# Kernel optimization log

Hardware: AMD Instinct MI355X
Metric: run time of the kernel (lower is better)

## Reference

```python
import jax, jax.numpy as jnp
import numpy as np
import math

B, T, C = 2, 2048, 2048
H, G, HS = 16, 4, 128  # n_head, n_query_groups, head_size
EPS = 1e-5
SCALE = 1.0 / math.sqrt(HS)
QKV_DIM = (H + 2 * G) * HS  # 3072, gate logits (H) appended after


def _build_rope(seq_len, n_elem, base):
    freq = base ** (np.arange(0, n_elem, 2, dtype=np.float64) / n_elem)
    inv_freq = 1.0 / freq
    idx_theta = np.outer(np.arange(seq_len, dtype=np.float64), inv_freq)
    return (jnp.asarray(np.cos(idx_theta), dtype=jnp.float32),
            jnp.asarray(np.sin(idx_theta), dtype=jnp.float32))


def setup_inputs() -> dict:
    key = jax.random.key(0)
    k1, k2, k3 = jax.random.split(key, 3)
    x = jax.random.normal(k1, (B, T, C), dtype=jnp.float32)
    # rope base per module: 0.09 * local_window ** 1.628
    base = 0.09 * (2048.0 ** 1.628)
    cos, sin = _build_rope(T, HS, base)  # [T, HS//2]
    W_attn = jax.random.normal(k2, (QKV_DIM + H, C), dtype=jnp.float32) * 0.02
    W_proj = jax.random.normal(k3, (C, H * HS), dtype=jnp.float32) * 0.02
    q_norm_w = jnp.ones((HS,), dtype=jnp.float32)
    k_norm_w = jnp.ones((HS,), dtype=jnp.float32)
    return {"x": x, "cos": cos, "sin": sin, "W_attn": W_attn,
            "q_norm_w": q_norm_w, "k_norm_w": k_norm_w, "W_proj": W_proj}


def _rms_norm(v, w):
    # per-head RMSNorm over last dim (head_size)
    ms = jnp.mean(jnp.square(v), axis=-1, keepdims=True)
    return v * jax.lax.rsqrt(ms + EPS) * w


def _apply_rope(v, cos, sin):
    # v: [B, T, N, HS]; cos/sin: [T, HS//2]; non-interleaved halves
    d2 = v.shape[-1] // 2
    x1, x2 = v[..., :d2], v[..., d2:]
    c = cos[None, :, None, :]
    s = sin[None, :, None, :]
    return jnp.concatenate([x1 * c - x2 * s, x2 * c + x1 * s], axis=-1)


def reference(x, cos, sin, W_attn, q_norm_w, k_norm_w, W_proj):
    qkv = jnp.einsum('btc,oc->bto', x, W_attn)  # [B, T, QKV_DIM+H]
    q = qkv[..., : H * HS].reshape(B, T, H, HS)
    k = qkv[..., H * HS:(H + G) * HS].reshape(B, T, G, HS)
    v = qkv[..., (H + G) * HS: QKV_DIM].reshape(B, T, G, HS)
    gate = qkv[..., QKV_DIM:]  # [B, T, H]

    q = _apply_rope(_rms_norm(q, q_norm_w), cos, sin)
    k = _apply_rope(_rms_norm(k, k_norm_w), cos, sin)

    rep = H // G
    kr = jnp.repeat(k, rep, axis=2)  # [B, T, H, HS]
    vr = jnp.repeat(v, rep, axis=2)

    scores = jnp.einsum('bthd,bshd->bhts', q, kr) * SCALE  # [B, H, T, T]
    causal = jnp.tril(jnp.ones((T, T), dtype=bool))
    scores = jnp.where(causal, scores, jnp.finfo(scores.dtype).min)
    probs = jax.nn.softmax(scores, axis=-1)
    out = jnp.einsum('bhts,bshd->bthd', probs, vr)  # [B, T, H, HS]

    out = out * jax.nn.sigmoid(gate)[..., None]  # gated attention, per-head
    y = jnp.einsum('bto,co->btc', out.reshape(B, T, H * HS), W_proj)
    return y
```

## Files before the change

### kernel.cpp

```cpp
#include <hip/hip_runtime.h>

#define T_   2048
#define BB   2
#define CC   2048
#define HH   16
#define GG   4
#define HSS  128
#define QKVD 3072
#define NQKV 3088
#define NPAD 3200
#define SCALE_ 0.08838834764831845f

typedef __attribute__((ext_vector_type(8))) short  short8;
typedef __attribute__((ext_vector_type(4))) float  f32x4;
typedef __attribute__((ext_vector_type(4))) int    v4i;
typedef __attribute__((ext_vector_type(4))) float  v4f;
typedef __attribute__((ext_vector_type(4))) unsigned short u16x4;

typedef const void __attribute__((address_space(1)))* gas1_t;
typedef void __attribute__((address_space(3)))* as3_t;

__device__ __forceinline__ void gl_lds16(const void* g, void* l) {
    __builtin_amdgcn_global_load_lds((gas1_t)g, (as3_t)l, 16, 0, 0);
}

__device__ __forceinline__ unsigned short f2bf(float f) {
    unsigned u = __float_as_uint(f);
    u += 0x7fffu + ((u >> 16) & 1u);
    return (unsigned short)(u >> 16);
}
__device__ __forceinline__ float bf2f(unsigned short h) {
    return __uint_as_float(((unsigned)h) << 16);
}

__global__ void k_convert(const float* __restrict__ src, unsigned short* __restrict__ dst,
                          int n_src4, int n_dst4) {
    int i = blockIdx.x * blockDim.x + threadIdx.x;
    if (i >= n_dst4) return;
    u16x4 o;
    if (i < n_src4) {
        v4f v = *(const v4f*)(src + (size_t)i * 4);
        o[0] = f2bf(v[0]); o[1] = f2bf(v[1]); o[2] = f2bf(v[2]); o[3] = f2bf(v[3]);
    } else {
        o[0] = 0; o[1] = 0; o[2] = 0; o[3] = 0;
    }
    *(u16x4*)(dst + (size_t)i * 4) = o;
}

template <typename OutT>
__launch_bounds__(512, 2)
__global__ void k_gemm8(const unsigned short* __restrict__ A,
                        const unsigned short* __restrict__ Bm,
                        OutT* __restrict__ C,
                        int K, int lda, int ldb, int ldc, int nmax) {
    __shared__ unsigned short As[2][256 * 64];
    __shared__ unsigned short Bs[2][256 * 64];
    const int t = threadIdx.x;
    const int lane = t & 63;
    const int wid  = t >> 6;
    const int wr = wid >> 2, wc = wid & 3;
    const int bm = blockIdx.x, bn = blockIdx.y;
    const int fro = lane & 15, fk = lane >> 4;

    const int srow  = lane >> 3;
    const size_t scol = (size_t)(((lane & 7) ^ srow) * 8);

    const unsigned short* Abase = A  + (size_t)(bm * 256) * lda;
    const unsigned short* Bbase = Bm + (size_t)(bn * 256) * ldb;

    f32x4 acc[8][4];
#pragma unroll
    for (int i = 0; i < 8; ++i)
#pragma unroll
        for (int j = 0; j < 4; ++j) acc[i][j] = (f32x4){0.f, 0.f, 0.f, 0.f};

#pragma unroll
    for (int h = 0; h < 2; ++h)
#pragma unroll
        for (int c8 = 0; c8 < 2; ++c8) {
            const int rr = h * 128 + wid * 16 + c8 * 8;
            gl_lds16(Abase + (size_t)(rr + srow) * lda + scol, &As[0][rr * 64]);
            gl_lds16(Bbase + (size_t)(rr + srow) * ldb + scol, &Bs[0][rr * 64]);
        }

    int cur = 0;
    for (int kt = 0; kt < K; kt += 64) {
        asm volatile("s_waitcnt vmcnt(0)" ::: "memory");
        __builtin_amdgcn_s_barrier();
        __builtin_amdgcn_sched_barrier(0);
        const bool pf = (kt + 64 < K);
        const int nxt = cur ^ 1;
        const int kn = kt + 64;

        short8 bf_[4][2];
#pragma unroll
        for (int q = 0; q < 4; ++q) {
            short8 af[2][2];
#pragma unroll
            for (int im = 0; im < 2; ++im)
#pragma unroll
                for (int kk = 0; kk < 2; ++kk) {
                    const int ar = wr * 128 + (q * 2 + im) * 16 + fro;
                    af[im][kk] = *(const short8*)&As[cur][ar * 64 + ((kk * 4 + fk) ^ (ar & 7)) * 8];
                }
            if (q == 0) {
#pragma unroll
                for (int ni = 0; ni < 4; ++ni)
#pragma unroll
                    for (int kk = 0; kk < 2; ++kk) {
                        const int br = wc * 64 + ni * 16 + fro;
                        bf_[ni][kk] = *(const short8*)&Bs[cur][br * 64 + ((kk * 4 + fk) ^ (br & 7)) * 8];
                    }
            }
            if (pf) {
                const int h = q & 1;
#pragma unroll
                for (int c8 = 0; c8 < 2; ++c8) {
                    const int rr = h * 128 + wid * 16 + c8 * 8;
                    if ((q >> 1) == 0)
                        gl_lds16(Abase + (size_t)(rr + srow) * lda + kn + scol, &As[nxt][rr * 64]);
                    else
                        gl_lds16(Bbase + (size_t)(rr + srow) * ldb + kn + scol, &Bs[nxt][rr * 64]);
                }
            }
            __builtin_amdgcn_s_setprio(1);
#pragma unroll
            for (int im = 0; im < 2; ++im)
#pragma unroll
                for (int ni = 0; ni < 4; ++ni)
#pragma unroll
                    for (int kk = 0; kk < 2; ++kk)
                        acc[q * 2 + im][ni] = __builtin_amdgcn_mfma_f32_16x16x32_bf16(
                            af[im][kk], bf_[ni][kk], acc[q * 2 + im][ni], 0, 0, 0);
            __builtin_amdgcn_s_setprio(0);
            __builtin_amdgcn_s_barrier();
        }
        cur ^= 1;
    }

    const int col16 = lane & 15, rbase = (lane >> 4) * 4;
    const int gr0 = bm * 256 + wr * 128;
    const int gc0 = bn * 256 + wc * 64;
#pragma unroll
    for (int mi = 0; mi < 8; ++mi)
#pragma unroll
        for (int ni = 0; ni < 4; ++ni) {
            const int gcol = gc0 + ni * 16 + col16;
            if (gcol < nmax) {
#pragma unroll
                for (int r = 0; r < 4; ++r) {
                    const int grow = gr0 + mi * 16 + rbase + r;
                    float v = acc[mi][ni][r];
                    if constexpr (sizeof(OutT) == 2)
                        C[(size_t)grow * ldc + gcol] = (OutT)f2bf(v);
                    else
                        C[(size_t)grow * ldc + gcol] = (OutT)v;
                }
            }
        }
}

__global__ void k_normrope(unsigned short* __restrict__ qkv,
                           const float* __restrict__ cosT, const float* __restrict__ sinT,
                           const float* __restrict__ qw, const float* __restrict__ kw) {
    const int lane = threadIdx.x & 63;
    const int row  = blockIdx.x * 4 + (threadIdx.x >> 6);
    const int tok  = row / 20;
    const int hh   = row - tok * 20;
    const int tpos = tok & (T_ - 1);
    unsigned short* rp = qkv + (size_t)tok * NPAD + (hh < 16 ? hh * 128 : 2048 + (hh - 16) * 128);
    const float* w = (hh < 16) ? qw : kw;
    float e1 = bf2f(rp[lane]);
    float e2 = bf2f(rp[lane + 64]);
    float ss = e1 * e1 + e2 * e2;
#pragma unroll
    for (int m = 1; m < 64; m <<= 1) ss += __shfl_xor(ss, m);
    float inv = rsqrtf(ss * (1.0f / 128.0f) + 1e-5f);
    float n1 = e1 * inv * w[lane];
    float n2 = e2 * inv * w[lane + 64];
    float c = cosT[tpos * 64 + lane];
    float s = sinT[tpos * 64 + lane];
    rp[lane]      = f2bf(n1 * c - n2 * s);
    rp[lane + 64] = f2bf(n2 * c + n1 * s);
}

__global__ void k_transposeV(const unsigned short* __restrict__ qkv,
                             unsigned short* __restrict__ vt) {
    __shared__ unsigned short tile[64][65];
    const int b = blockIdx.x >> 2, g = blockIdx.x & 3;
    const int s0 = blockIdx.y * 64, d0 = blockIdx.z * 64;
    const int tx = threadIdx.x & 63, ty0 = threadIdx.x >> 6;
    const unsigned short* src = qkv + (size_t)(b * T_ + s0) * NPAD + 2560 + g * 128 + d0;
#pragma unroll
    for (int r = 0; r < 16; ++r) {
        int ty = ty0 * 16 + r;
        tile[ty][tx] = src[(size_t)ty * NPAD + tx];
    }
    __syncthreads();
    unsigned short* dstp = vt + ((size_t)(b * GG + g) * 128 + d0) * T_ + s0;
#pragma unroll
    for (int r = 0; r < 16; ++r) {
        int ty = ty0 * 16 + r;
        dstp[(size_t)ty * T_ + tx] = tile[tx][ty];
    }
}

__launch_bounds__(256, 2)
__global__ void k_attn(const unsigned short* __restrict__ qkv,
                       const unsigned short* __restrict__ vt,
                       unsigned short* __restrict__ ao) {
    __shared__ unsigned short Ks[2][64 * 128];
    __shared__ unsigned short Vs[2][128 * 64];
    __shared__ unsigned short Ps[4][16 * 72];
    const int t = threadIdx.x;
    const int lane = t & 63;
    const int wid  = t >> 6;
    const int id = blockIdx.x;
    const int bg = id & 7;
    const int hh = (id >> 3) & 3;
    const int pr = id >> 5;
    const int b = bg >> 2, g = bg & 3, h = g * 4 + hh;
    const int fro = lane & 15, fk = lane >> 4;
    const int rbase = fk * 4;

    const unsigned short* kg0 = qkv + (size_t)(b * T_) * NPAD + 2048 + g * 128;
    const unsigned short* vg0 = vt + (size_t)(b * GG + g) * 128 * T_;

    const int cp0 = wid * 4;
    int cur = 0;

#pragma unroll
    for (int seg = 0; seg < 2; ++seg) {
        const int qt = (seg == 0) ? pr : 31 - pr;
        const int q0w = qt * 64 + wid * 16;

        short8 qf[4];
        const unsigned short* qp = qkv + (size_t)(b * T_ + q0w + fro) * NPAD + h * 128 + fk * 8;
#pragma unroll
        for (int kb = 0; kb < 4; ++kb) qf[kb] = *(const short8*)(qp + kb * 32);

        float m_r[4], l_r[4];
        f32x4 o[8];
#pragma unroll
        for (int r = 0; r < 4; ++r) { m_r[r] = -1e30f; l_r[r] = 0.f; }
#pragma unroll
        for (int d = 0; d < 8; ++d) o[d] = (f32x4){0.f, 0.f, 0.f, 0.f};

        const int nt = qt + 1;

#pragma unroll
        for (int p = 0; p < 4; ++p) {
            const int cp = cp0 + p;
            const int kr = cp * 4 + (lane >> 4);
            const int sK = lane & 15;
            gl_lds16(kg0 + (size_t)kr * NPAD + (size_t)((sK ^ (kr & 7)) * 8), &Ks[cur][cp * 512]);
            const int d  = cp * 8 + (lane >> 3);
            const int sV = lane & 7;
            gl_lds16(vg0 + (size_t)d * T_ + (size_t)((sV ^ (d & 7)) * 8), &Vs[cur][cp * 512]);
        }
        __syncthreads();

        for (int ti = 0; ti < nt; ++ti) {
            if (ti + 1 < nt) {
                const int sn = (ti + 1) * 64;
#pragma unroll
                for (int p = 0; p < 4; ++p) {
                    const int cp = cp0 + p;
                    const int kr = cp * 4 + (lane >> 4);
                    const int sK = lane & 15;
                    gl_lds16(kg0 + (size_t)(sn + kr) * NPAD + (size_t)((sK ^ (kr & 7)) * 8), &Ks[cur ^ 1][cp * 512]);
                    const int d  = cp * 8 + (lane >> 3);
                    const int sV = lane & 7;
                    gl_lds16(vg0 + (size_t)d * T_ + sn + (size_t)((sV ^ (d & 7)) * 8), &Vs[cur ^ 1][cp * 512]);
                }
            }
            f32x4 sc[4];
#pragma unroll
            for (int jb = 0; jb < 4; ++jb) sc[jb] = (f32x4){0.f, 0.f, 0.f, 0.f};
#pragma unroll
            for (int jb = 0; jb < 4; ++jb) {
                const int kr = jb * 16 + fro;
#pragma unroll
                for (int kb = 0; kb < 4; ++kb) {
                    short8 kf = *(const short8*)&Ks[cur][kr * 128 + 8 * ((kb * 4 + fk) ^ (kr & 7))];
                    sc[jb] = __builtin_amdgcn_mfma_f32_16x16x32_bf16(qf[kb], kf, sc[jb], 0, 0, 0);
                }
            }
            const bool domask = (ti == qt);
#pragma unroll
            for (int jb = 0; jb < 4; ++jb)
#pragma unroll
                for (int r = 0; r < 4; ++r) {
                    float v = sc[jb][r] * SCALE_;
                    if (domask && (jb * 16 + fro) > (wid * 16 + rbase + r)) v = -1e30f;
                    sc[jb][r] = v;
                }
            float mx[4], fs[4], rs[4];
#pragma unroll
            for (int r = 0; r < 4; ++r)
                mx[r] = fmaxf(fmaxf(sc[0][r], sc[1][r]), fmaxf(sc[2][r], sc[3][r]));
#pragma unroll
            for (int msk = 1; msk < 16; msk <<= 1)
#pragma unroll
                for (int r = 0; r < 4; ++r) mx[r] = fmaxf(mx[r], __shfl_xor(mx[r], msk));
#pragma unroll
            for (int r = 0; r < 4; ++r) {
                float mn = fmaxf(m_r[r], mx[r]);
                fs[r] = __expf(m_r[r] - mn);
                m_r[r] = mn;
            }
#pragma unroll
            for (int jb = 0; jb < 4; ++jb)
#pragma unroll
                for (int r = 0; r < 4; ++r) sc[jb][r] = __expf(sc[jb][r] - m_r[r]);
#pragma unroll
            for (int r = 0; r < 4; ++r)
                rs[r] = (sc[0][r] + sc[1][r]) + (sc[2][r] + sc[3][r]);
#pragma unroll
            for (int msk = 1; msk < 16; msk <<= 1)
#pragma unroll
                for (int r = 0; r < 4; ++r) rs[r] += __shfl_xor(rs[r], msk);
#pragma unroll
            for (int r = 0; r < 4; ++r) l_r[r] = l_r[r] * fs[r] + rs[r];
#pragma unroll
            for (int d = 0; d < 8; ++d)
#pragma unroll
                for (int r = 0; r < 4; ++r) o[d][r] *= fs[r];
            unsigned short* pw = &Ps[wid][0];
#pragma unroll
            for (int jb = 0; jb < 4; ++jb)
#pragma unroll
                for (int r = 0; r < 4; ++r)
                    pw[(rbase + r) * 72 + jb * 16 + fro] = f2bf(sc[jb][r]);
            asm volatile("s_waitcnt lgkmcnt(0)" ::: "memory");
            __builtin_amdgcn_sched_barrier(0);
            short8 pa[2];
#pragma unroll
            for (int ks = 0; ks < 2; ++ks)
                pa[ks] = *(const short8*)&Ps[wid][fro * 72 + ks * 32 + fk * 8];
#pragma unroll
            for (int ks = 0; ks < 2; ++ks)
#pragma unroll
                for (int db = 0; db < 8; ++db) {
                    const int d = db * 16 + fro;
                    short8 vf = *(const short8*)&Vs[cur][d * 64 + 8 * ((ks * 4 + fk) ^ (d & 7))];
                    o[db] = __builtin_amdgcn_mfma_f32_16x16x32_bf16(pa[ks], vf, o[db], 0, 0, 0);
                }
            __syncthreads();
            cur ^= 1;
        }
#pragma unroll
        for (int r = 0; r < 4; ++r) {
            const int qrow = q0w + rbase + r;
            float gv = bf2f(qkv[(size_t)(b * T_ + qrow) * NPAD + QKVD + h]);
            float sg = 1.f / (1.f + __expf(-gv));
            float invl = sg / l_r[r];
            unsigned short* orow = ao + (size_t)(b * T_ + qrow) * 2048 + h * 128;
#pragma unroll
            for (int db = 0; db < 8; ++db)
                orow[db * 16 + fro] = f2bf(o[db][r] * invl);
        }
    }
}

extern "C" void kernel_launch(void* const* d_in, const int* in_sizes, int n_in,
                              void* d_out, int out_size, void* d_ws, size_t ws_size,
                              hipStream_t stream) {
    const float* x      = (const float*)d_in[0];
    const float* cosT   = (const float*)d_in[1];
    const float* sinT   = (const float*)d_in[2];
    const float* W_attn = (const float*)d_in[3];
    const float* qw     = (const float*)d_in[4];
    const float* kw     = (const float*)d_in[5];
    const float* W_proj = (const float*)d_in[6];

    char* ws = (char*)d_ws;
    const size_t OFF_XB   = 0;
    const size_t OFF_WAB  = 16777216;
    const size_t OFF_WPB  = 29884416;
    const size_t OFF_QKV  = 38273024;
    const size_t OFF_VT   = 64487424;
    const size_t OFF_AO   = 68681728;
    const size_t NEED     = 85458944;
    if (ws_size < NEED) return;

    unsigned short* xb   = (unsigned short*)(ws + OFF_XB);
    unsigned short* wab  = (unsigned short*)(ws + OFF_WAB);
    unsigned short* wpb  = (unsigned short*)(ws + OFF_WPB);
    unsigned short* qkvb = (unsigned short*)(ws + OFF_QKV);
    unsigned short* vtb  = (unsigned short*)(ws + OFF_VT);
    unsigned short* aob  = (unsigned short*)(ws + OFF_AO);

    k_convert<<<8192, 256, 0, stream>>>(x,      xb,  2097152, 2097152);
    k_convert<<<6400, 256, 0, stream>>>(W_attn, wab, 1581056, 1638400);
    k_convert<<<4096, 256, 0, stream>>>(W_proj, wpb, 1048576, 1048576);
    k_gemm8<unsigned short><<<dim3(16, 13), 512, 0, stream>>>(xb, wab, qkvb, 2048, 2048, 2048, NPAD, NPAD);
    k_normrope<<<20480, 256, 0, stream>>>(qkvb, cosT, sinT, qw, kw);
    k_transposeV<<<dim3(8, 32, 2), 256, 0, stream>>>(qkvb, vtb);
    k_attn<<<512, 256, 0, stream>>>(qkvb, vtb, aob);
    k_gemm8<float><<<dim3(16, 8), 512, 0, stream>>>(aob, wpb, (float*)d_out, 2048, 2048, 2048, 2048, 2048);
}
```

Baseline: 246.3 us.

## Add BM template to GEMM, use 128-row tiles for output projection, DPP softmax reductions

```diff
diff --git a/kernel.cpp b/kernel.cpp
--- a/kernel.cpp
+++ b/kernel.cpp
@@ -10,6 +10,7 @@
 #define NQKV 3088
 #define NPAD 3200
 #define SCALE_ 0.08838834764831845f
+#define SCALE2_ (0.08838834764831845f * 1.4426950408889634f)
 
 typedef __attribute__((ext_vector_type(8))) short  short8;
 typedef __attribute__((ext_vector_type(4))) float  f32x4;
@@ -31,6 +32,32 @@
 }
 __device__ __forceinline__ float bf2f(unsigned short h) {
     return __uint_as_float(((unsigned)h) << 16);
+}
+
+template <int CTRL>
+__device__ __forceinline__ float dppmv(float x) {
+    int i = __float_as_int(x);
+    return __int_as_float(__builtin_amdgcn_update_dpp(i, i, CTRL, 0xF, 0xF, false));
+}
+__device__ __forceinline__ void red16_max(float* v) {
+#pragma unroll
+    for (int r = 0; r < 4; ++r) v[r] = fmaxf(v[r], dppmv<0xB1>(v[r]));
+#pragma unroll
+    for (int r = 0; r < 4; ++r) v[r] = fmaxf(v[r], dppmv<0x4E>(v[r]));
+#pragma unroll
+    for (int r = 0; r < 4; ++r) v[r] = fmaxf(v[r], dppmv<0x124>(v[r]));
+#pragma unroll
+    for (int r = 0; r < 4; ++r) v[r] = fmaxf(v[r], dppmv<0x128>(v[r]));
+}
+__device__ __forceinline__ void red16_sum(float* v) {
+#pragma unroll
+    for (int r = 0; r < 4; ++r) v[r] += dppmv<0xB1>(v[r]);
+#pragma unroll
+    for (int r = 0; r < 4; ++r) v[r] += dppmv<0x4E>(v[r]);
+#pragma unroll
+    for (int r = 0; r < 4; ++r) v[r] += dppmv<0x124>(v[r]);
+#pragma unroll
+    for (int r = 0; r < 4; ++r) v[r] += dppmv<0x128>(v[r]);
 }
 
 __global__ void k_convert(const float* __restrict__ src, unsigned short* __restrict__ dst,
@@ -47,13 +74,15 @@
     *(u16x4*)(dst + (size_t)i * 4) = o;
 }
 
-template <typename OutT>
+template <int BM_, typename OutT>
 __launch_bounds__(512, 2)
 __global__ void k_gemm8(const unsigned short* __restrict__ A,
                         const unsigned short* __restrict__ Bm,
                         OutT* __restrict__ C,
                         int K, int lda, int ldb, int ldc, int nmax) {
-    __shared__ unsigned short As[2][256 * 64];
+    constexpr int MI  = BM_ / 32;
+    constexpr int NPH = MI / 2;
+    __shared__ unsigned short As[2][BM_ * 64];
     __shared__ unsigned short Bs[2][256 * 64];
     const int t = threadIdx.x;
     const int lane = t & 63;
@@ -65,12 +94,12 @@
     const int srow  = lane >> 3;
     const size_t scol = (size_t)(((lane & 7) ^ srow) * 8);
 
-    const unsigned short* Abase = A  + (size_t)(bm * 256) * lda;
+    const unsigned short* Abase = A  + (size_t)(bm * BM_) * lda;
     const unsigned short* Bbase = Bm + (size_t)(bn * 256) * ldb;
 
-    f32x4 acc[8][4];
-#pragma unroll
-    for (int i = 0; i < 8; ++i)
+    f32x4 acc[MI][4];
+#pragma unroll
+    for (int i = 0; i < MI; ++i)
 #pragma unroll
         for (int j = 0; j < 4; ++j) acc[i][j] = (f32x4){0.f, 0.f, 0.f, 0.f};
 
@@ -79,7 +108,8 @@
 #pragma unroll
         for (int c8 = 0; c8 < 2; ++c8) {
             const int rr = h * 128 + wid * 16 + c8 * 8;
-            gl_lds16(Abase + (size_t)(rr + srow) * lda + scol, &As[0][rr * 64]);
+            if (BM_ == 256 || h == 0)
+                gl_lds16(Abase + (size_t)(rr + srow) * lda + scol, &As[0][rr * 64]);
             gl_lds16(Bbase + (size_t)(rr + srow) * ldb + scol, &Bs[0][rr * 64]);
         }
 
@@ -94,13 +124,13 @@
 
         short8 bf_[4][2];
 #pragma unroll
-        for (int q = 0; q < 4; ++q) {
+        for (int q = 0; q < NPH; ++q) {
             short8 af[2][2];
 #pragma unroll
             for (int im = 0; im < 2; ++im)
 #pragma unroll
                 for (int kk = 0; kk < 2; ++kk) {
-                    const int ar = wr * 128 + (q * 2 + im) * 16 + fro;
+                    const int ar = wr * (BM_ / 2) + (q * 2 + im) * 16 + fro;
                     af[im][kk] = *(const short8*)&As[cur][ar * 64 + ((kk * 4 + fk) ^ (ar & 7)) * 8];
                 }
             if (q == 0) {
@@ -113,14 +143,32 @@
                     }
             }
             if (pf) {
-                const int h = q & 1;
-#pragma unroll
-                for (int c8 = 0; c8 < 2; ++c8) {
-                    const int rr = h * 128 + wid * 16 + c8 * 8;
-                    if ((q >> 1) == 0)
-                        gl_lds16(Abase + (size_t)(rr + srow) * lda + kn + scol, &As[nxt][rr * 64]);
-                    else
-                        gl_lds16(Bbase + (size_t)(rr + srow) * ldb + kn + scol, &Bs[nxt][rr * 64]);
+                if (BM_ == 256) {
+                    const int h = q & 1;
+#pragma unroll
+                    for (int c8 = 0; c8 < 2; ++c8) {
+                        const int rr = h * 128 + wid * 16 + c8 * 8;
+                        if ((q >> 1) == 0)
+                            gl_lds16(Abase + (size_t)(rr + srow) * lda + kn + scol, &As[nxt][rr * 64]);
+                        else
+                            gl_lds16(Bbase + (size_t)(rr + srow) * ldb + kn + scol, &Bs[nxt][rr * 64]);
+                    }
+                } else {
+                    if (q == 0) {
+#pragma unroll
+                        for (int c8 = 0; c8 < 2; ++c8) {
+                            const int rr = wid * 16 + c8 * 8;
+                            gl_lds16(Abase + (size_t)(rr + srow) * lda + kn + scol, &As[nxt][rr * 64]);
+                        }
+                    } else {
+#pragma unroll
+                        for (int h = 0; h < 2; ++h)
+#pragma unroll
+                            for (int c8 = 0; c8 < 2; ++c8) {
+                                const int rr = h * 128 + wid * 16 + c8 * 8;
+                                gl_lds16(Bbase + (size_t)(rr + srow) * ldb + kn + scol, &Bs[nxt][rr * 64]);
+                            }
+                    }
                 }
             }
             __builtin_amdgcn_s_setprio(1);
@@ -139,10 +187,10 @@
     }
 
     const int col16 = lane & 15, rbase = (lane >> 4) * 4;
-    const int gr0 = bm * 256 + wr * 128;
+    const int gr0 = bm * BM_ + wr * (BM_ / 2);
     const int gc0 = bn * 256 + wc * 64;
 #pragma unroll
-    for (int mi = 0; mi < 8; ++mi)
+    for (int mi = 0; mi < MI; ++mi)
 #pragma unroll
         for (int ni = 0; ni < 4; ++ni) {
             const int gcol = gc0 + ni * 16 + col16;
@@ -291,7 +339,7 @@
             for (int jb = 0; jb < 4; ++jb)
 #pragma unroll
                 for (int r = 0; r < 4; ++r) {
-                    float v = sc[jb][r] * SCALE_;
+                    float v = sc[jb][r] * SCALE2_;
                     if (domask && (jb * 16 + fro) > (wid * 16 + rbase + r)) v = -1e30f;
                     sc[jb][r] = v;
                 }
@@ -299,27 +347,21 @@
 #pragma unroll
             for (int r = 0; r < 4; ++r)
                 mx[r] = fmaxf(fmaxf(sc[0][r], sc[1][r]), fmaxf(sc[2][r], sc[3][r]));
-#pragma unroll
-            for (int msk = 1; msk < 16; msk <<= 1)
-#pragma unroll
-                for (int r = 0; r < 4; ++r) mx[r] = fmaxf(mx[r], __shfl_xor(mx[r], msk));
+            red16_max(mx);
 #pragma unroll
             for (int r = 0; r < 4; ++r) {
                 float mn = fmaxf(m_r[r], mx[r]);
-                fs[r] = __expf(m_r[r] - mn);
+                fs[r] = exp2f(m_r[r] - mn);
                 m_r[r] = mn;
             }
 #pragma unroll
             for (int jb = 0; jb < 4; ++jb)
 #pragma unroll
-                for (int r = 0; r < 4; ++r) sc[jb][r] = __expf(sc[jb][r] - m_r[r]);
+                for (int r = 0; r < 4; ++r) sc[jb][r] = exp2f(sc[jb][r] - m_r[r]);
 #pragma unroll
             for (int r = 0; r < 4; ++r)
                 rs[r] = (sc[0][r] + sc[1][r]) + (sc[2][r] + sc[3][r]);
-#pragma unroll
-            for (int msk = 1; msk < 16; msk <<= 1)
-#pragma unroll
-                for (int r = 0; r < 4; ++r) rs[r] += __shfl_xor(rs[r], msk);
+            red16_sum(rs);
 #pragma unroll
             for (int r = 0; r < 4; ++r) l_r[r] = l_r[r] * fs[r] + rs[r];
 #pragma unroll
@@ -394,9 +436,9 @@
     k_convert<<<8192, 256, 0, stream>>>(x,      xb,  2097152, 2097152);
     k_convert<<<6400, 256, 0, stream>>>(W_attn, wab, 1581056, 1638400);
     k_convert<<<4096, 256, 0, stream>>>(W_proj, wpb, 1048576, 1048576);
-    k_gemm8<unsigned short><<<dim3(16, 13), 512, 0, stream>>>(xb, wab, qkvb, 2048, 2048, 2048, NPAD, NPAD);
+    k_gemm8<256, unsigned short><<<dim3(16, 13), 512, 0, stream>>>(xb, wab, qkvb, 2048, 2048, 2048, NPAD, NPAD);
     k_normrope<<<20480, 256, 0, stream>>>(qkvb, cosT, sinT, qw, kw);
     k_transposeV<<<dim3(8, 32, 2), 256, 0, stream>>>(qkvb, vtb);
     k_attn<<<512, 256, 0, stream>>>(qkvb, vtb, aob);
-    k_gemm8<float><<<dim3(16, 8), 512, 0, stream>>>(aob, wpb, (float*)d_out, 2048, 2048, 2048, 2048, 2048);
-}
+    k_gemm8<128, float><<<dim3(32, 8), 512, 0, stream>>>(aob, wpb, (float*)d_out, 2048, 2048, 2048, 2048, 2048);
+}
```

New measurement: 224.4 us. -8.9%, faster.
